# Optimization experiments

Measured on AMD Instinct MI355X. Metric: run time of the kernel, lower is better.

The kernel has to match this reference:

```python
import jax, jax.numpy as jnp
import numpy as np

N, T, E, V, ED, DD, H = 50000, 8, 800000, 1000, 16, 32, 128
G0 = 2 * ED + DD  # GNN input dim = 64


def setup_inputs() -> dict:
    key = jax.random.key(0)
    ks = jax.random.split(key, 20)
    s = 0.05  # init scale for stability
    return {
        "static_dense_x": jax.random.normal(ks[0], (N, DD), jnp.float32),
        "static_sparse_x": jax.random.randint(ks[1], (N, 2), 0, V, jnp.int32),
        "dynamic_dense_x": jax.random.normal(ks[2], (T, N, DD), jnp.float32),
        "dynamic_sparse_x": jax.random.randint(ks[3], (T, N, 2), 0, V, jnp.int32),
        "edges": jax.random.randint(ks[4], (T, 2, E), 0, N, jnp.int32),
        "weights": jax.random.uniform(ks[5], (T, E), jnp.float32),
        "static_emb": jax.random.normal(ks[6], (2, V, ED), jnp.float32) * s,
        "dynamic_emb": jax.random.normal(ks[7], (2, V, ED), jnp.float32) * s,
        "Ws": jax.random.normal(ks[8], (G0, H), jnp.float32) * s,
        "bs": jnp.zeros((H,), jnp.float32),
        "gW1": jax.random.normal(ks[9], (T, G0, H), jnp.float32) * s,
        "gb1": jnp.zeros((T, H), jnp.float32),
        "gW2": jax.random.normal(ks[10], (T, H, H), jnp.float32) * s,
        "gb2": jnp.zeros((T, H), jnp.float32),
        "Wx": jax.random.normal(ks[11], (H, 3 * H), jnp.float32) * s,
        "Wh": jax.random.normal(ks[12], (H, 3 * H), jnp.float32) * s,
        "bx": jnp.zeros((3 * H,), jnp.float32),
        "bh": jnp.zeros((3 * H,), jnp.float32),
        "Waw": jax.random.normal(ks[13], (H, 1), jnp.float32) * s,
        "baw": jnp.zeros((1,), jnp.float32),
    }


def _forward(static_dense_x, dynamic_dense_x, weights, static_emb, dynamic_emb,
             Ws, bs, gW1, gb1, gW2, gb2, Wx, Wh, bx, bh, Waw, baw,
             static_sparse_x, dynamic_sparse_x, edges):
    n = static_dense_x.shape[0]
    h_dim = Wh.shape[0]
    # Embedding layer: concat sparse embeddings with dense features
    static_x = jnp.concatenate(
        [static_emb[0][static_sparse_x[:, 0]], static_emb[1][static_sparse_x[:, 1]], static_dense_x], -1)  # [N, 64]
    static_embed = jax.nn.relu(static_x @ Ws + bs)  # MLP static encoder -> [N, H]
    dyn_x = jnp.concatenate(
        [dynamic_emb[0][dynamic_sparse_x[:, :, 0]], dynamic_emb[1][dynamic_sparse_x[:, :, 1]], dynamic_dense_x], -1)  # [T, N, 64]

    def gcn(x, e, w, W1, b1, W2, b2):
        # weighted message aggregation (src -> dst) then linear, two layers
        m1 = jax.ops.segment_sum(w[:, None] * x[e[0]], e[1], num_segments=n)
        h1 = jax.nn.relu(m1 @ W1 + b1)
        m2 = jax.ops.segment_sum(w[:, None] * h1[e[0]], e[1], num_segments=n)
        return m2 @ W2 + b2

    g = jax.vmap(gcn)(dyn_x, edges, weights, gW1, gb1, gW2, gb2)  # [T, N, H]

    def gru_step(h, x):
        gx = x @ Wx + bx
        gh = h @ Wh + bh
        xr, xz, xn = jnp.split(gx, 3, -1)
        hr, hz, hn = jnp.split(gh, 3, -1)
        r = jax.nn.sigmoid(xr + hr)
        z = jax.nn.sigmoid(xz + hz)
        ncand = jnp.tanh(xn + r * hn)
        h_new = (1.0 - z) * ncand + z * h
        return h_new, h_new

    h0 = jnp.zeros((n, h_dim), g.dtype)
    _, hs = jax.lax.scan(gru_step, h0, g)  # [T, N, H]

    embed = jnp.concatenate([static_embed[None], hs], 0)  # [T+1, N, H]
    att = jax.nn.softmax(jnp.tanh(embed) @ Waw + baw, axis=0)  # softmax over time
    return jnp.sum(embed * att, axis=0)  # [N, H]


def reference(static_dense_x, static_sparse_x, dynamic_dense_x, dynamic_sparse_x, edges, weights,
              static_emb, dynamic_emb, Ws, bs, gW1, gb1, gW2, gb2, Wx, Wh, bx, bh, Waw, baw):
    return _forward(static_dense_x, dynamic_dense_x, weights, static_emb, dynamic_emb,
                    Ws, bs, gW1, gb1, gW2, gb2, Wx, Wh, bx, bh, Waw, baw,
                    static_sparse_x, dynamic_sparse_x, edges)
```

## Files before the change

### kernel.cpp

```cpp
#include <hip/hip_runtime.h>
#include <hip/hip_bf16.h>
#include <string.h>

#define NNODES 50000
#define TSTEPS 8
#define NEDGES 800000
#define VVOCAB 1000
#define DDIM 32
#define HDIM 128
#define G0DIM 64
#define H3 384
#define NSB 4
#define SRCBLK 12500
#define NKEY (NNODES * NSB)
#define NBLK 256
#define EPB 3125
#define COARSE 391
#define FINEN 512
#define NSCN (COARSE * NBLK)
#define NCHK2 196
#define STAGE_CAP 4096

typedef _Float16 v8h __attribute__((ext_vector_type(8)));
typedef float v4f __attribute__((ext_vector_type(4)));

__device__ __forceinline__ float w_decode(unsigned int packed) {
  unsigned short wb = (unsigned short)(packed >> 16);
  _Float16 h;
  __builtin_memcpy(&h, &wb, 2);
  return (float)h;
}

__device__ __forceinline__ float fsigmoid(float v) {
  return __builtin_amdgcn_rcpf(1.f + __expf(-v));
}
__device__ __forceinline__ float ftanh(float x) {
  float xc = fminf(fmaxf(x, -15.f), 15.f);
  float e2 = __expf(2.f * xc);
  return (e2 - 1.f) * __builtin_amdgcn_rcpf(e2 + 1.f);
}


__global__ __launch_bounds__(512) void coarse_hist(const int* __restrict__ edges,
                                                   int* __restrict__ bh) {
  __shared__ int hist[COARSE];
  int t = blockIdx.y, b = blockIdx.x, tid = threadIdx.x;
  for (int i = tid; i < COARSE; i += 512) hist[i] = 0;
  __syncthreads();
  const int* srcp = edges + (size_t)t * 2 * NEDGES + (size_t)b * EPB;
  const int* dstp = srcp + NEDGES;
  for (int i = tid; i < EPB; i += 512) {
    int key = dstp[i] * NSB + srcp[i] / SRCBLK;
    atomicAdd(&hist[key >> 9], 1);
  }
  __syncthreads();
  for (int i = tid; i < COARSE; i += 512) bh[(size_t)t * NSCN + i * NBLK + b] = hist[i];
}

__global__ __launch_bounds__(256) void scan_c1(const int* __restrict__ bh,
                                               int* __restrict__ csum) {
  int bid = blockIdx.x;
  int t = bid / NCHK2, c = bid % NCHK2;
  int tid = threadIdx.x;
  int s = 0;
#pragma unroll
  for (int i = 0; i < 2; ++i) {
    int n = c * 512 + tid + i * 256;
    if (n < NSCN) s += bh[(size_t)t * NSCN + n];
  }
#pragma unroll
  for (int off = 32; off > 0; off >>= 1) s += __shfl_down(s, off, 64);
  __shared__ int wsum[4];
  if ((tid & 63) == 0) wsum[tid >> 6] = s;
  __syncthreads();
  if (tid == 0) csum[bid] = wsum[0] + wsum[1] + wsum[2] + wsum[3];
}

__global__ __launch_bounds__(512) void scan_c2(const int* __restrict__ csum,
                                               int* __restrict__ cbase) {
  int t = blockIdx.x;
  int tid = threadIdx.x;
  __shared__ int buf[512];
  int own = (tid < NCHK2) ? csum[t * NCHK2 + tid] : 0;
  buf[tid] = own;
  __syncthreads();
  for (int d = 1; d < 512; d <<= 1) {
    int v = (tid >= d) ? buf[tid - d] : 0;
    __syncthreads();
    buf[tid] += v;
    __syncthreads();
  }
  if (tid < NCHK2) cbase[t * NCHK2 + tid] = buf[tid] - own;
}

__global__ __launch_bounds__(512) void scan_c3(const int* __restrict__ bh,
                                               const int* __restrict__ cbase,
                                               int* __restrict__ bscan) {
  int bid = blockIdx.x;
  int t = bid / NCHK2, c = bid % NCHK2;
  int tid = threadIdx.x;
  int n = c * 512 + tid;
  int d = (n < NSCN) ? bh[(size_t)t * NSCN + n] : 0;
  __shared__ int buf[512];
  buf[tid] = d;
  __syncthreads();
  for (int s = 1; s < 512; s <<= 1) {
    int v = (tid >= s) ? buf[tid - s] : 0;
    __syncthreads();
    buf[tid] += v;
    __syncthreads();
  }
  if (n < NSCN) bscan[(size_t)t * NSCN + n] = cbase[bid] + buf[tid] - d;
}

__global__ __launch_bounds__(512) void coarse_scatter(
    const int* __restrict__ edges, const float* __restrict__ weights,
    const int* __restrict__ bscan, int2* __restrict__ tmp) {
  __shared__ int hist[COARSE], lstart[COARSE], cur[COARSE], scanb[COARSE];
  __shared__ int2 stage[EPB];
  __shared__ unsigned short binof[EPB];
  int t = blockIdx.y, b = blockIdx.x, tid = threadIdx.x;
  for (int i = tid; i < COARSE; i += 512) hist[i] = 0;
  __syncthreads();
  const int* srcp = edges + (size_t)t * 2 * NEDGES + (size_t)b * EPB;
  const int* dstp = srcp + NEDGES;
  const float* wp = weights + (size_t)t * NEDGES + (size_t)b * EPB;
  for (int i = tid; i < EPB; i += 512) {
    int key = dstp[i] * NSB + srcp[i] / SRCBLK;
    atomicAdd(&hist[key >> 9], 1);
  }
  __syncthreads();
  if (tid < COARSE) scanb[tid] = hist[tid];
  __syncthreads();
  for (int d = 1; d < COARSE; d <<= 1) {
    int v = 0;
    if (tid < COARSE && tid >= d) v = scanb[tid - d];
    __syncthreads();
    if (tid < COARSE) scanb[tid] += v;
    __syncthreads();
  }
  if (tid < COARSE) {
    int ls = scanb[tid] - hist[tid];
    lstart[tid] = ls;
    cur[tid] = ls;
  }
  __syncthreads();
  for (int i = tid; i < EPB; i += 512) {
    int src = srcp[i];
    int key = dstp[i] * NSB + src / SRCBLK;
    int coarse = key >> 9, fine = key & 511;
    int lpos = atomicAdd(&cur[coarse], 1);
    int2 pk;
    pk.x = src | (fine << 16);
    pk.y = __float_as_int(wp[i]);
    stage[lpos] = pk;
    binof[lpos] = (unsigned short)coarse;
  }
  __syncthreads();
  for (int j = tid; j < EPB; j += 512) {
    int lo = binof[j];
    int gpos = bscan[(size_t)t * NSCN + lo * NBLK + b] + (j - lstart[lo]);
    tmp[(size_t)t * NEDGES + gpos] = stage[j];
  }
}

__global__ __launch_bounds__(512) void fine_sort(
    const int* __restrict__ bscan, const int2* __restrict__ tmp,
    unsigned int* __restrict__ csr, int* __restrict__ offs) {
  __shared__ int fhist[FINEN], fbase[FINEN], fcur[FINEN], buf[FINEN];
  __shared__ unsigned int stage[STAGE_CAP];
  int t = blockIdx.y, coarse = blockIdx.x, tid = threadIdx.x;
  int cb0 = bscan[(size_t)t * NSCN + coarse * NBLK];
  int cb1 = (coarse == COARSE - 1) ? NEDGES : bscan[(size_t)t * NSCN + (coarse + 1) * NBLK];
  int size = cb1 - cb0;
  fhist[tid] = 0;
  fcur[tid] = 0;
  __syncthreads();
  const int2* bin = tmp + (size_t)t * NEDGES + cb0;
  for (int i = tid; i < size; i += 512) {
    int fine = (bin[i].x >> 16) & 511;
    atomicAdd(&fhist[fine], 1);
  }
  __syncthreads();
  buf[tid] = fhist[tid];
  __syncthreads();
  for (int d = 1; d < FINEN; d <<= 1) {
    int v = (tid >= d) ? buf[tid - d] : 0;
    __syncthreads();
    buf[tid] += v;
    __syncthreads();
  }
  fbase[tid] = buf[tid] - fhist[tid];
  int key = coarse * FINEN + tid;
  if (key < NKEY) offs[(size_t)t * (NKEY + 1) + key] = cb0 + fbase[tid];
  if (coarse == COARSE - 1 && tid == 0) offs[(size_t)t * (NKEY + 1) + NKEY] = NEDGES;
  __syncthreads();
  unsigned int* outp = csr + (size_t)t * NEDGES + cb0;
  if (size <= STAGE_CAP) {
    for (int i = tid; i < size; i += 512) {
      int2 p = bin[i];
      int fine = (p.x >> 16) & 511;
      int lr = atomicAdd(&fcur[fine], 1);
      _Float16 wh = (_Float16)__int_as_float(p.y);
      unsigned short wb;
      __builtin_memcpy(&wb, &wh, 2);
      stage[fbase[fine] + lr] = (unsigned int)(p.x & 0xFFFF) | ((unsigned int)wb << 16);
    }
    __syncthreads();
    for (int i = tid; i < size; i += 512) outp[i] = stage[i];
  } else {
    for (int i = tid; i < size; i += 512) {
      int2 p = bin[i];
      int fine = (p.x >> 16) & 511;
      int lr = atomicAdd(&fcur[fine], 1);
      _Float16 wh = (_Float16)__int_as_float(p.y);
      unsigned short wb;
      __builtin_memcpy(&wb, &wh, 2);
      outp[fbase[fine] + lr] = (unsigned int)(p.x & 0xFFFF) | ((unsigned int)wb << 16);
    }
  }
}


template <int D>
__global__ __launch_bounds__(256) void gather_merged(
    const int* __restrict__ off, const unsigned int* __restrict__ csr,
    const _Float16* __restrict__ x, _Float16* __restrict__ m) {
  const int LPN = D / 8;
  int n = blockIdx.x * (256 / LPN) + threadIdx.x / LPN;
  int l = threadIdx.x % LPN;
  if (n >= NNODES) return;
  int s0 = off[n * NSB], s1 = off[(n + 1) * NSB];
  float a0[8], a1[8];
#pragma unroll
  for (int i = 0; i < 8; ++i) { a0[i] = 0.f; a1[i] = 0.f; }
  int e = s0;
  for (; e + 1 < s1; e += 2) {
    unsigned int eA = csr[e], eB = csr[e + 1];
    v8h xA = *(const v8h*)&x[(size_t)(eA & 0xFFFF) * D + l * 8];
    v8h xB = *(const v8h*)&x[(size_t)(eB & 0xFFFF) * D + l * 8];
    float wA = w_decode(eA), wB = w_decode(eB);
#pragma unroll
    for (int i = 0; i < 8; ++i) {
      a0[i] += wA * (float)xA[i];
      a1[i] += wB * (float)xB[i];
    }
  }
  if (e < s1) {
    unsigned int eA = csr[e];
    v8h xA = *(const v8h*)&x[(size_t)(eA & 0xFFFF) * D + l * 8];
    float wA = w_decode(eA);
#pragma unroll
    for (int i = 0; i < 8; ++i) a0[i] += wA * (float)xA[i];
  }
  v8h r;
#pragma unroll
  for (int i = 0; i < 8; ++i) r[i] = (_Float16)(a0[i] + a1[i]);
  *(v8h*)&m[(size_t)n * D + l * 8] = r;
}


__global__ __launch_bounds__(384) void fuse_w(
    const float* __restrict__ gW2, const float* __restrict__ Wx, float* __restrict__ Wf) {
  int t = blockIdx.x >> 7;
  int k = blockIdx.x & 127;
  int j = threadIdx.x;
  __shared__ float row[HDIM];
  if (j < HDIM) row[j] = gW2[((size_t)t * HDIM + k) * HDIM + j];
  __syncthreads();
  float acc = 0.f;
#pragma unroll 8
  for (int c = 0; c < HDIM; ++c) acc += row[c] * Wx[c * H3 + j];
  Wf[((size_t)t * HDIM + k) * H3 + j] = acc;
}

__global__ __launch_bounds__(384) void fuse_b(
    const float* __restrict__ gb2, const float* __restrict__ Wx,
    const float* __restrict__ bx, float* __restrict__ bf) {
  int t = blockIdx.x;
  int j = threadIdx.x;
  __shared__ float row[HDIM];
  if (j < HDIM) row[j] = gb2[t * HDIM + j];
  __syncthreads();
  float acc = bx[j];
#pragma unroll 8
  for (int c = 0; c < HDIM; ++c) acc += row[c] * Wx[c * H3 + j];
  bf[t * H3 + j] = acc;
}

__global__ __launch_bounds__(256) void pack_wcomb(
    const float* __restrict__ Wf32, const float* __restrict__ Wh,
    _Float16* __restrict__ Bp) {
  int t = blockIdx.x >> 9;
  int col = blockIdx.x & 511;
  int k = threadIdx.x;
  float v;
  if (col < 384) {
    if (k < 128) v = Wf32[((size_t)t * HDIM + k) * H3 + col];
    else v = (col < 256) ? Wh[(size_t)(k - 128) * H3 + col] : 0.f;
  } else {
    v = (k < 128) ? 0.f : Wh[(size_t)(k - 128) * H3 + (col - 128)];
  }
  int cg = col >> 4, lj = col & 15;
  int ks = k >> 5, rem = k & 31, lr = rem >> 3, ki = rem & 7;
  size_t idx = ((((((size_t)t * 8 + ks) * 32 + cg) * 4 + lr) * 16 + lj) * 8) + ki;
  Bp[idx] = (_Float16)v;
}

__global__ __launch_bounds__(512) void pack_bcomb(
    const float* __restrict__ bfb, const float* __restrict__ bh,
    float* __restrict__ bcomb) {
  int t = blockIdx.x;
  int c = threadIdx.x;
  float v;
  if (c < 256) v = bfb[t * H3 + c] + bh[c];
  else if (c < 384) v = bfb[t * H3 + c];
  else v = bh[c - 128];
  bcomb[t * 512 + c] = v;
}

__global__ __launch_bounds__(64) void static_encode8(
    const float* __restrict__ dense, const int* __restrict__ sparse,
    const float* __restrict__ emb,
    const float* __restrict__ Ws, const float* __restrict__ bs,
    const float* __restrict__ Waw, const float* __restrict__ baw,
    _Float16* __restrict__ acch, float* __restrict__ s, float* __restrict__ mx) {
  const int NB = 8;
  int n0 = blockIdx.x * NB;
  int j = threadIdx.x;
  __shared__ float xT[G0DIM][NB + 1];
#pragma unroll
  for (int q = 0; q < NB; ++q) {
    int n = n0 + q;
    float v = 0.f;
    if (n < NNODES) {
      if (j < 16) v = emb[sparse[n * 2 + 0] * 16 + j];
      else if (j < 32) v = emb[VVOCAB * 16 + sparse[n * 2 + 1] * 16 + (j - 16)];
      else v = dense[(size_t)n * DDIM + (j - 32)];
    }
    xT[j][q] = v;
  }
  __syncthreads();
  float acc0[NB], acc1[NB];
#pragma unroll
  for (int q = 0; q < NB; ++q) { acc0[q] = 0.f; acc1[q] = 0.f; }
#pragma unroll 4
  for (int k = 0; k < G0DIM; ++k) {
    float w0 = Ws[(size_t)k * HDIM + j];
    float w1 = Ws[(size_t)k * HDIM + j + 64];
#pragma unroll
    for (int q = 0; q < NB; ++q) {
      float xv = xT[k][q];
      acc0[q] += xv * w0;
      acc1[q] += xv * w1;
    }
  }
  float b0 = bs[j], b1 = bs[j + 64];
  float waw0 = Waw[j], waw1 = Waw[j + 64];
#pragma unroll
  for (int q = 0; q < NB; ++q) {
    int n = n0 + q;
    float a0 = fmaxf(acc0[q] + b0, 0.f);
    float a1 = fmaxf(acc1[q] + b1, 0.f);
    if (n < NNODES) {
      acch[(size_t)n * HDIM + j] = (_Float16)a0;
      acch[(size_t)n * HDIM + j + 64] = (_Float16)a1;
    }
    float v = ftanh(a0) * waw0 + ftanh(a1) * waw1;
#pragma unroll
    for (int off = 32; off > 0; off >>= 1) v += __shfl_down(v, off, 64);
    if (j == 0 && n < NNODES) {
      s[n] = 1.f;
      mx[n] = v + baw[0];
    }
  }
}

__global__ __launch_bounds__(256) void dynx_gather_h(
    const float* __restrict__ dense_t, const int* __restrict__ sparse_t,
    const float* __restrict__ emb, _Float16* __restrict__ xout) {
  int idx = blockIdx.x * 256 + threadIdx.x;
  int n = idx >> 3, k8 = idx & 7;
  if (n >= NNODES) return;
  const float* src;
  if (k8 < 2)
    src = &emb[sparse_t[n * 2 + 0] * 16 + k8 * 8];
  else if (k8 < 4)
    src = &emb[VVOCAB * 16 + sparse_t[n * 2 + 1] * 16 + (k8 - 2) * 8];
  else
    src = &dense_t[n * DDIM + (k8 - 4) * 8];
  float4 f0 = *(const float4*)src;
  float4 f1 = *(const float4*)(src + 4);
  v8h v = {(_Float16)f0.x, (_Float16)f0.y, (_Float16)f0.z, (_Float16)f0.w,
           (_Float16)f1.x, (_Float16)f1.y, (_Float16)f1.z, (_Float16)f1.w};
  *(v8h*)&xout[(size_t)n * G0DIM + k8 * 8] = v;
}

__global__ __launch_bounds__(64) void rowmm64(
    const _Float16* __restrict__ x, const float* __restrict__ W,
    const float* __restrict__ b, _Float16* __restrict__ y) {
  const int NB = 8;
  int n0 = blockIdx.x * NB;
  int j = threadIdx.x;
  __shared__ float xT[G0DIM][12];
#pragma unroll
  for (int q = 0; q < NB; ++q) xT[j][q] = (float)x[(size_t)(n0 + q) * G0DIM + j];
  __syncthreads();
  float acc0[NB], acc1[NB];
#pragma unroll
  for (int q = 0; q < NB; ++q) { acc0[q] = 0.f; acc1[q] = 0.f; }
#pragma unroll 4
  for (int k = 0; k < G0DIM; ++k) {
    float4 a = *(const float4*)&xT[k][0];
    float4 c = *(const float4*)&xT[k][4];
    float w0 = W[(size_t)k * HDIM + j];
    float w1 = W[(size_t)k * HDIM + j + 64];
    acc0[0] += a.x * w0; acc0[1] += a.y * w0; acc0[2] += a.z * w0; acc0[3] += a.w * w0;
    acc0[4] += c.x * w0; acc0[5] += c.y * w0; acc0[6] += c.z * w0; acc0[7] += c.w * w0;
    acc1[0] += a.x * w1; acc1[1] += a.y * w1; acc1[2] += a.z * w1; acc1[3] += a.w * w1;
    acc1[4] += c.x * w1; acc1[5] += c.y * w1; acc1[6] += c.z * w1; acc1[7] += c.w * w1;
  }
  float b0 = b[j], b1 = b[j + 64];
#pragma unroll
  for (int q = 0; q < NB; ++q) {
    y[(size_t)(n0 + q) * HDIM + j] = (_Float16)fmaxf(acc0[q] + b0, 0.f);
    y[(size_t)(n0 + q) * HDIM + j + 64] = (_Float16)fmaxf(acc1[q] + b1, 0.f);
  }
}

__global__ __launch_bounds__(512) void gru_mfma(
    const _Float16* __restrict__ Xh, const _Float16* __restrict__ Hp,
    const _Float16* __restrict__ Bt, const float* __restrict__ bcomb,
    const float* __restrict__ Waw, const float* __restrict__ baw,
    _Float16* __restrict__ hout, _Float16* __restrict__ acch,
    float* __restrict__ outf, float* __restrict__ sden, float* __restrict__ mxv,
    int last) {
  const int AST = 264;
  __shared__ _Float16 A_lds[64 * AST];
  __shared__ _Float16 h_lds[64 * 132];
  __shared__ float lg[64], facs[64], ps[64], sdn[64];
  int tid = threadIdx.x;
  int w = tid >> 6, lane = tid & 63;
  int n0 = blockIdx.x * 64;

#pragma unroll
  for (int i = 0; i < 4; ++i) {
    int cid = tid + i * 512;
    int row = cid >> 5, ch = cid & 31;
    int n = n0 + row;
    v8h v = {(_Float16)0, (_Float16)0, (_Float16)0, (_Float16)0,
             (_Float16)0, (_Float16)0, (_Float16)0, (_Float16)0};
    if (n < NNODES) {
      if (ch < 16) v = *(const v8h*)&Xh[(size_t)n * HDIM + ch * 8];
      else if (Hp) v = *(const v8h*)&Hp[(size_t)n * HDIM + (ch - 16) * 8];
    }
    *(v8h*)&A_lds[row * AST + ch * 8] = v;
  }
  __syncthreads();

  int lj = lane & 15, lr = lane >> 4;
  const v8h* Bp = (const v8h*)Bt;
  v4f accf[4][4];
#pragma unroll
  for (int m = 0; m < 4; ++m)
#pragma unroll
    for (int g = 0; g < 4; ++g) accf[m][g] = (v4f){0.f, 0.f, 0.f, 0.f};

  for (int ks = 0; ks < 8; ++ks) {
    v8h a0 = *(const v8h*)&A_lds[(0 + lj) * AST + ks * 32 + lr * 8];
    v8h a1 = *(const v8h*)&A_lds[(16 + lj) * AST + ks * 32 + lr * 8];
    v8h a2 = *(const v8h*)&A_lds[(32 + lj) * AST + ks * 32 + lr * 8];
    v8h a3 = *(const v8h*)&A_lds[(48 + lj) * AST + ks * 32 + lr * 8];
#pragma unroll
    for (int g = 0; g < 4; ++g) {
      int cg = g * 8 + w;
      v8h b = Bp[((ks * 32 + cg) * 4 + lr) * 16 + lj];
      accf[0][g] = __builtin_amdgcn_mfma_f32_16x16x32_f16(a0, b, accf[0][g], 0, 0, 0);
      accf[1][g] = __builtin_amdgcn_mfma_f32_16x16x32_f16(a1, b, accf[1][g], 0, 0, 0);
      accf[2][g] = __builtin_amdgcn_mfma_f32_16x16x32_f16(a2, b, accf[2][g], 0, 0, 0);
      accf[3][g] = __builtin_amdgcn_mfma_f32_16x16x32_f16(a3, b, accf[3][g], 0, 0, 0);
    }
  }

  {
    int j = w * 16 + lj;
    float br = bcomb[j], bz = bcomb[128 + j], bxn = bcomb[256 + j], bhn = bcomb[384 + j];
#pragma unroll
    for (int m = 0; m < 4; ++m)
#pragma unroll
      for (int reg = 0; reg < 4; ++reg) {
        int row = m * 16 + lr * 4 + reg;
        float r = fsigmoid(accf[m][0][reg] + br);
        float z = fsigmoid(accf[m][1][reg] + bz);
        float hp = (float)A_lds[row * AST + 128 + j];
        float nc = ftanh(accf[m][2][reg] + bxn + r * (accf[m][3][reg] + bhn));
        h_lds[row * 132 + j] = (_Float16)((1.f - z) * nc + z * hp);
      }
  }
  __syncthreads();

  float waw0 = Waw[lane], waw1 = Waw[lane + 64];
#pragma unroll
  for (int q = 0; q < 8; ++q) {
    int row = w * 8 + q;
    float v = ftanh((float)h_lds[row * 132 + lane]) * waw0 +
              ftanh((float)h_lds[row * 132 + lane + 64]) * waw1;
#pragma unroll
    for (int off = 32; off > 0; off >>= 1) v += __shfl_down(v, off, 64);
    if (lane == 0) lg[row] = v;
  }
  __syncthreads();
  if (tid < 64) {
    int n = n0 + tid;
    if (n < NNODES) {
      float l = lg[tid] + baw[0];
      float m = mxv[n];
      float mnew = fmaxf(m, l);
      float fac = __expf(m - mnew);
      float pp = __expf(l - mnew);
      facs[tid] = fac;
      ps[tid] = pp;
      float snew = sden[n] * fac + pp;
      sdn[tid] = snew;
      sden[n] = snew;
      mxv[n] = mnew;
    }
  }
  __syncthreads();
  if (last) {
#pragma unroll
    for (int i = 0; i < 16; ++i) {
      int idx = tid + i * 512;
      int row = idx >> 7, col = idx & 127;
      int n = n0 + row;
      if (n < NNODES) {
        float hv = (float)h_lds[row * 132 + col];
        size_t o = (size_t)n * HDIM + col;
        float av = (float)acch[o];
        outf[o] = (av * facs[row] + ps[row] * hv) / sdn[row];
      }
    }
  } else {
#pragma unroll
    for (int i = 0; i < 16; ++i) {
      int idx = tid + i * 512;
      int row = idx >> 7, col = idx & 127;
      int n = n0 + row;
      if (n < NNODES) {
        float hv = (float)h_lds[row * 132 + col];
        size_t o = (size_t)n * HDIM + col;
        float av = (float)acch[o];
        acch[o] = (_Float16)(av * facs[row] + ps[row] * hv);
        hout[o] = (_Float16)hv;
      }
    }
  }
}

extern "C" void kernel_launch(void* const* d_in, const int* in_sizes, int n_in,
                              void* d_out, int out_size, void* d_ws, size_t ws_size,
                              hipStream_t stream) {
  const float* static_dense = (const float*)d_in[0];
  const int*   static_sparse = (const int*)d_in[1];
  const float* dyn_dense = (const float*)d_in[2];
  const int*   dyn_sparse = (const int*)d_in[3];
  const int*   edges = (const int*)d_in[4];
  const float* weights = (const float*)d_in[5];
  const float* s_emb = (const float*)d_in[6];
  const float* d_emb = (const float*)d_in[7];
  const float* Ws = (const float*)d_in[8];
  const float* bs = (const float*)d_in[9];
  const float* gW1 = (const float*)d_in[10];
  const float* gb1 = (const float*)d_in[11];
  const float* gW2 = (const float*)d_in[12];
  const float* gb2 = (const float*)d_in[13];
  const float* Wx = (const float*)d_in[14];
  const float* Wh = (const float*)d_in[15];
  const float* bx = (const float*)d_in[16];
  const float* bh_in = (const float*)d_in[17];
  const float* Waw = (const float*)d_in[18];
  const float* baw = (const float*)d_in[19];
  float* out = (float*)d_out;

  const size_t N = NNODES;
  char* p = (char*)d_ws;
  auto alloc = [&](size_t bytes) { char* r = p; p += (bytes + 255) & ~(size_t)255; return r; };
  float*     sden   = (float*)alloc(N * 4);
  float*     mxv    = (float*)alloc(N * 4);
  _Float16*  acch   = (_Float16*)alloc(N * HDIM * 2);
  char*      big    = alloc(64UL * 1024 * 1024);
  _Float16*  hA     = (_Float16*)big;
  _Float16*  hB     = hA + N * HDIM;
  _Float16*  dynx   = hB + N * HDIM;
  _Float16*  m1h    = dynx + N * G0DIM;
  _Float16*  h1h    = m1h + N * G0DIM;
  _Float16*  Xh     = h1h + N * HDIM;
  int2*      tmp    = (int2*)big;
  float*     Wf32   = (float*)alloc((size_t)TSTEPS * HDIM * H3 * 4);
  _Float16*  Wcombt = (_Float16*)alloc((size_t)TSTEPS * 512 * 256 * 2);
  float*     bfb    = (float*)alloc((size_t)TSTEPS * H3 * 4);
  float*     bcomb  = (float*)alloc((size_t)TSTEPS * 512 * 4);
  int*       bhist  = (int*)alloc((size_t)TSTEPS * NSCN * 4);
  int*       bscan  = (int*)alloc((size_t)TSTEPS * NSCN * 4);
  int*       csum   = (int*)alloc((size_t)TSTEPS * NCHK2 * 4);
  int*       cbase  = (int*)alloc((size_t)TSTEPS * NCHK2 * 4);
  int*       offs   = (int*)alloc((size_t)TSTEPS * (NKEY + 1) * 4);
  unsigned int* csr = (unsigned int*)alloc((size_t)TSTEPS * NEDGES * 4);

  coarse_hist<<<dim3(NBLK, TSTEPS), 512, 0, stream>>>(edges, bhist);
  scan_c1<<<TSTEPS * NCHK2, 256, 0, stream>>>(bhist, csum);
  scan_c2<<<TSTEPS, 512, 0, stream>>>(csum, cbase);
  scan_c3<<<TSTEPS * NCHK2, 512, 0, stream>>>(bhist, cbase, bscan);
  coarse_scatter<<<dim3(NBLK, TSTEPS), 512, 0, stream>>>(edges, weights, bscan, tmp);
  fine_sort<<<dim3(COARSE, TSTEPS), 512, 0, stream>>>(bscan, tmp, csr, offs);

  fuse_w<<<TSTEPS * HDIM, H3, 0, stream>>>(gW2, Wx, Wf32);
  fuse_b<<<TSTEPS, H3, 0, stream>>>(gb2, Wx, bx, bfb);
  pack_wcomb<<<TSTEPS * 512, 256, 0, stream>>>(Wf32, Wh, Wcombt);
  pack_bcomb<<<TSTEPS, 512, 0, stream>>>(bfb, bh_in, bcomb);

  static_encode8<<<(NNODES + 7) / 8, 64, 0, stream>>>(
      static_dense, static_sparse, s_emb, Ws, bs, Waw, baw, acch, sden, mxv);

  const int GRUB = (NNODES + 63) / 64;
  for (int t = 0; t < TSTEPS; ++t) {
    const int* off_t = offs + (size_t)t * (NKEY + 1);
    const unsigned int* csr_t = csr + (size_t)t * NEDGES;
    _Float16* hcur = (t & 1) ? hB : hA;
    const _Float16* hprev = (t == 0) ? nullptr : ((t & 1) ? hA : hB);

    dynx_gather_h<<<(NNODES * 8 + 255) / 256, 256, 0, stream>>>(
        dyn_dense + (size_t)t * N * DDIM, dyn_sparse + (size_t)t * N * 2, d_emb, dynx);

    gather_merged<G0DIM><<<(NNODES + 31) / 32, 256, 0, stream>>>(off_t, csr_t, dynx, m1h);

    rowmm64<<<NNODES / 8, 64, 0, stream>>>(
        m1h, gW1 + (size_t)t * G0DIM * HDIM, gb1 + (size_t)t * HDIM, h1h);

    gather_merged<HDIM><<<(NNODES + 15) / 16, 256, 0, stream>>>(off_t, csr_t, h1h, Xh);

    gru_mfma<<<GRUB, 512, 0, stream>>>(
        Xh, hprev, Wcombt + (size_t)t * 512 * 256, bcomb + t * 512,
        Waw, baw, hcur, acch, out, sden, mxv, t == TSTEPS - 1 ? 1 : 0);
  }
}
```

Measured before the change: 980.2 us.

## Fuse first GCN gather with 64x128 matmul and unroll 128-wide gather

Merges the 64-dim edge aggregation and the following dense layer (W1, bias, ReLU) into one kernel. The aggregated rows stay in shared memory instead of going through an fp16 buffer in global memory, and one launch per step is dropped. The 128-wide gather now processes four edges per iteration instead of two to keep more loads in flight. The fused kernel also keeps the aggregate in fp32 rather than rounding it to fp16 first, which slightly changes numerics. The larger block and bigger shared tile may lower occupancy.

```diff
diff --git a/kernel.cpp b/kernel.cpp
--- a/kernel.cpp
+++ b/kernel.cpp
@@ -222,33 +222,33 @@
 }
 
 
-template <int D>
-__global__ __launch_bounds__(256) void gather_merged(
+__global__ __launch_bounds__(256) void gather128(
     const int* __restrict__ off, const unsigned int* __restrict__ csr,
     const _Float16* __restrict__ x, _Float16* __restrict__ m) {
-  const int LPN = D / 8;
-  int n = blockIdx.x * (256 / LPN) + threadIdx.x / LPN;
-  int l = threadIdx.x % LPN;
+  int n = blockIdx.x * 16 + (threadIdx.x >> 4);
+  int l = threadIdx.x & 15;
   if (n >= NNODES) return;
   int s0 = off[n * NSB], s1 = off[(n + 1) * NSB];
   float a0[8], a1[8];
 #pragma unroll
   for (int i = 0; i < 8; ++i) { a0[i] = 0.f; a1[i] = 0.f; }
   int e = s0;
-  for (; e + 1 < s1; e += 2) {
-    unsigned int eA = csr[e], eB = csr[e + 1];
-    v8h xA = *(const v8h*)&x[(size_t)(eA & 0xFFFF) * D + l * 8];
-    v8h xB = *(const v8h*)&x[(size_t)(eB & 0xFFFF) * D + l * 8];
-    float wA = w_decode(eA), wB = w_decode(eB);
+  for (; e + 3 < s1; e += 4) {
+    unsigned int e0 = csr[e], e1 = csr[e + 1], e2 = csr[e + 2], e3 = csr[e + 3];
+    v8h x0 = *(const v8h*)&x[(size_t)(e0 & 0xFFFF) * HDIM + l * 8];
+    v8h x1 = *(const v8h*)&x[(size_t)(e1 & 0xFFFF) * HDIM + l * 8];
+    v8h x2 = *(const v8h*)&x[(size_t)(e2 & 0xFFFF) * HDIM + l * 8];
+    v8h x3 = *(const v8h*)&x[(size_t)(e3 & 0xFFFF) * HDIM + l * 8];
+    float w0 = w_decode(e0), w1 = w_decode(e1), w2 = w_decode(e2), w3 = w_decode(e3);
 #pragma unroll
     for (int i = 0; i < 8; ++i) {
-      a0[i] += wA * (float)xA[i];
-      a1[i] += wB * (float)xB[i];
-    }
-  }
-  if (e < s1) {
+      a0[i] += w0 * (float)x0[i] + w2 * (float)x2[i];
+      a1[i] += w1 * (float)x1[i] + w3 * (float)x3[i];
+    }
+  }
+  for (; e < s1; ++e) {
     unsigned int eA = csr[e];
-    v8h xA = *(const v8h*)&x[(size_t)(eA & 0xFFFF) * D + l * 8];
+    v8h xA = *(const v8h*)&x[(size_t)(eA & 0xFFFF) * HDIM + l * 8];
     float wA = w_decode(eA);
 #pragma unroll
     for (int i = 0; i < 8; ++i) a0[i] += wA * (float)xA[i];
@@ -256,7 +256,70 @@
   v8h r;
 #pragma unroll
   for (int i = 0; i < 8; ++i) r[i] = (_Float16)(a0[i] + a1[i]);
-  *(v8h*)&m[(size_t)n * D + l * 8] = r;
+  *(v8h*)&m[(size_t)n * HDIM + l * 8] = r;
+}
+
+__global__ __launch_bounds__(256) void gcn1_fused(
+    const int* __restrict__ off, const unsigned int* __restrict__ csr,
+    const _Float16* __restrict__ x, const float* __restrict__ W,
+    const float* __restrict__ b, _Float16* __restrict__ y) {
+  __shared__ float xT[G0DIM][33];
+  int tid = threadIdx.x;
+  int n0 = blockIdx.x * 32;
+  {
+    int q = tid >> 3, l = tid & 7;
+    int n = n0 + q;
+    float a0[8];
+#pragma unroll
+    for (int i = 0; i < 8; ++i) a0[i] = 0.f;
+    if (n < NNODES) {
+      int s0 = off[n * NSB], s1 = off[(n + 1) * NSB];
+      int e = s0;
+      for (; e + 1 < s1; e += 2) {
+        unsigned int eA = csr[e], eB = csr[e + 1];
+        v8h xA = *(const v8h*)&x[(size_t)(eA & 0xFFFF) * G0DIM + l * 8];
+        v8h xB = *(const v8h*)&x[(size_t)(eB & 0xFFFF) * G0DIM + l * 8];
+        float wA = w_decode(eA), wB = w_decode(eB);
+#pragma unroll
+        for (int i = 0; i < 8; ++i) a0[i] += wA * (float)xA[i] + wB * (float)xB[i];
+      }
+      if (e < s1) {
+        unsigned int eA = csr[e];
+        v8h xA = *(const v8h*)&x[(size_t)(eA & 0xFFFF) * G0DIM + l * 8];
+        float wA = w_decode(eA);
+#pragma unroll
+        for (int i = 0; i < 8; ++i) a0[i] += wA * (float)xA[i];
+      }
+    }
+#pragma unroll
+    for (int i = 0; i < 8; ++i) xT[l * 8 + i][q] = a0[i];
+  }
+  __syncthreads();
+  int g2 = tid >> 6, j = tid & 63;
+  int qb = g2 * 8;
+  float acc0[8], acc1[8];
+#pragma unroll
+  for (int q = 0; q < 8; ++q) { acc0[q] = 0.f; acc1[q] = 0.f; }
+#pragma unroll 4
+  for (int k = 0; k < G0DIM; ++k) {
+    float w0 = W[(size_t)k * HDIM + j];
+    float w1 = W[(size_t)k * HDIM + j + 64];
+#pragma unroll
+    for (int q = 0; q < 8; ++q) {
+      float xv = xT[k][qb + q];
+      acc0[q] += xv * w0;
+      acc1[q] += xv * w1;
+    }
+  }
+  float b0 = b[j], b1 = b[j + 64];
+#pragma unroll
+  for (int q = 0; q < 8; ++q) {
+    int n = n0 + qb + q;
+    if (n < NNODES) {
+      y[(size_t)n * HDIM + j] = (_Float16)fmaxf(acc0[q] + b0, 0.f);
+      y[(size_t)n * HDIM + j + 64] = (_Float16)fmaxf(acc1[q] + b1, 0.f);
+    }
+  }
 }
 
 
@@ -394,38 +457,6 @@
   v8h v = {(_Float16)f0.x, (_Float16)f0.y, (_Float16)f0.z, (_Float16)f0.w,
            (_Float16)f1.x, (_Float16)f1.y, (_Float16)f1.z, (_Float16)f1.w};
   *(v8h*)&xout[(size_t)n * G0DIM + k8 * 8] = v;
-}
-
-__global__ __launch_bounds__(64) void rowmm64(
-    const _Float16* __restrict__ x, const float* __restrict__ W,
-    const float* __restrict__ b, _Float16* __restrict__ y) {
-  const int NB = 8;
-  int n0 = blockIdx.x * NB;
-  int j = threadIdx.x;
-  __shared__ float xT[G0DIM][12];
-#pragma unroll
-  for (int q = 0; q < NB; ++q) xT[j][q] = (float)x[(size_t)(n0 + q) * G0DIM + j];
-  __syncthreads();
-  float acc0[NB], acc1[NB];
-#pragma unroll
-  for (int q = 0; q < NB; ++q) { acc0[q] = 0.f; acc1[q] = 0.f; }
-#pragma unroll 4
-  for (int k = 0; k < G0DIM; ++k) {
-    float4 a = *(const float4*)&xT[k][0];
-    float4 c = *(const float4*)&xT[k][4];
-    float w0 = W[(size_t)k * HDIM + j];
-    float w1 = W[(size_t)k * HDIM + j + 64];
-    acc0[0] += a.x * w0; acc0[1] += a.y * w0; acc0[2] += a.z * w0; acc0[3] += a.w * w0;
-    acc0[4] += c.x * w0; acc0[5] += c.y * w0; acc0[6] += c.z * w0; acc0[7] += c.w * w0;
-    acc1[0] += a.x * w1; acc1[1] += a.y * w1; acc1[2] += a.z * w1; acc1[3] += a.w * w1;
-    acc1[4] += c.x * w1; acc1[5] += c.y * w1; acc1[6] += c.z * w1; acc1[7] += c.w * w1;
-  }
-  float b0 = b[j], b1 = b[j + 64];
-#pragma unroll
-  for (int q = 0; q < NB; ++q) {
-    y[(size_t)(n0 + q) * HDIM + j] = (_Float16)fmaxf(acc0[q] + b0, 0.f);
-    y[(size_t)(n0 + q) * HDIM + j + 64] = (_Float16)fmaxf(acc1[q] + b1, 0.f);
-  }
 }
 
 __global__ __launch_bounds__(512) void gru_mfma(
@@ -592,8 +623,7 @@
   _Float16*  hA     = (_Float16*)big;
   _Float16*  hB     = hA + N * HDIM;
   _Float16*  dynx   = hB + N * HDIM;
-  _Float16*  m1h    = dynx + N * G0DIM;
-  _Float16*  h1h    = m1h + N * G0DIM;
+  _Float16*  h1h    = dynx + N * G0DIM;
   _Float16*  Xh     = h1h + N * HDIM;
   int2*      tmp    = (int2*)big;
   float*     Wf32   = (float*)alloc((size_t)TSTEPS * HDIM * H3 * 4);
@@ -632,12 +662,10 @@
     dynx_gather_h<<<(NNODES * 8 + 255) / 256, 256, 0, stream>>>(
         dyn_dense + (size_t)t * N * DDIM, dyn_sparse + (size_t)t * N * 2, d_emb, dynx);
 
-    gather_merged<G0DIM><<<(NNODES + 31) / 32, 256, 0, stream>>>(off_t, csr_t, dynx, m1h);
-
-    rowmm64<<<NNODES / 8, 64, 0, stream>>>(
-        m1h, gW1 + (size_t)t * G0DIM * HDIM, gb1 + (size_t)t * HDIM, h1h);
-
-    gather_merged<HDIM><<<(NNODES + 15) / 16, 256, 0, stream>>>(off_t, csr_t, h1h, Xh);
+    gcn1_fused<<<(NNODES + 31) / 32, 256, 0, stream>>>(
+        off_t, csr_t, dynx, gW1 + (size_t)t * G0DIM * HDIM, gb1 + (size_t)t * HDIM, h1h);
+
+    gather128<<<(NNODES + 15) / 16, 256, 0, stream>>>(off_t, csr_t, h1h, Xh);
 
     gru_mfma<<<GRUB, 512, 0, stream>>>(
         Xh, hprev, Wcombt + (size_t)t * 512 * 256, bcomb + t * 512,
```

Result: faster. 954.5 us (-2.6%).
